# Kernel optimization log

Measured on AMD Instinct MI355X. Metric: run time of the kernel, lower is better.

Reference implementation:

```python
import jax, jax.numpy as jnp
import numpy as np

B, S, N, BS, D, H, V = 1, 2048, 128, 16, 512, 8, 32000
MASK_TOKEN_ID = 3


def setup_inputs() -> dict:
    key = jax.random.key(0)
    ks = jax.random.split(key, 10)
    anchors = jnp.sort(jax.random.randint(ks[0], (B, N), 0, S - BS), axis=1)
    return {
        "input_ids": jax.random.randint(ks[1], (B, S), 0, V),
        "hidden_states": jax.random.normal(ks[2], (B, S, D), dtype=jnp.float32),
        "loss_mask": jnp.ones((B, S), dtype=jnp.float32),
        "anchor_positions": anchors,
        "block_keep_mask": jnp.ones((B, N), dtype=bool),
        "embed_table": jax.random.normal(ks[3], (V, D), dtype=jnp.float32) * 0.02,
        "Wq": jax.random.normal(ks[4], (D, D), dtype=jnp.float32) * 0.02,
        "Wk": jax.random.normal(ks[5], (D, D), dtype=jnp.float32) * 0.02,
        "Wv": jax.random.normal(ks[6], (D, D), dtype=jnp.float32) * 0.02,
        "Wo": jax.random.normal(ks[7], (D, D), dtype=jnp.float32) * 0.02,
        "W_lm": jax.random.normal(ks[8], (D, V), dtype=jnp.float32) * 0.02,
    }


def dflash_sdpa_mask(anchor_positions, block_keep_mask):
    # KV layout: [context S | block_0 .. block_{N-1}], Q layout: [block_0 .. block_{N-1}]
    Q = N * BS
    KV = S + N * BS
    q_idx = jnp.arange(Q)              # [Q]
    kv_idx = jnp.arange(KV)            # [KV]
    q_blk = q_idx // BS                # [Q]
    anchor_q = anchor_positions[:, q_blk]          # [B,Q] anchor of each query's block
    keep_q = block_keep_mask[:, q_blk]             # [B,Q]
    is_ctx = kv_idx < S                             # [KV]
    mask_context = is_ctx[None, None, :] & (kv_idx[None, None, :] < anchor_q[:, :, None])  # [B,Q,KV]
    kv_blk = (kv_idx - S) // BS
    mask_draft = (kv_idx >= S)[None, :] & (q_blk[:, None] == kv_blk[None, :])              # [Q,KV]
    final = (mask_context | mask_draft[None]) & keep_q[:, :, None]                          # [B,Q,KV]
    return final


def reference(input_ids, hidden_states, loss_mask, anchor_positions, block_keep_mask,
              embed_table, Wq, Wk, Wv, Wo, W_lm):
    dh = D // H
    Q = N * BS

    # --- noise embedding: MASK token everywhere, anchor token at each block start ---
    safe_anchor = jnp.clip(anchor_positions, 0, S - 1)                     # [B,N]
    anchor_tokens = jnp.take_along_axis(input_ids, safe_anchor, axis=1)    # [B,N]
    start_tokens = jnp.where(block_keep_mask, anchor_tokens, MASK_TOKEN_ID)
    noise_ids = jnp.full((B, Q), MASK_TOKEN_ID, dtype=input_ids.dtype)
    noise_ids = noise_ids.at[:, jnp.arange(N) * BS].set(start_tokens)
    noise_embedding = embed_table[noise_ids]                               # [B,Q,D]

    # --- draft attention: Q = draft tokens, KV = [context hiddens | draft tokens] ---
    kv_in = jnp.concatenate([hidden_states, noise_embedding], axis=1)      # [B,S+Q,D]
    q = (noise_embedding @ Wq).reshape(B, Q, H, dh)
    k = (kv_in @ Wk).reshape(B, S + Q, H, dh)
    v = (kv_in @ Wv).reshape(B, S + Q, H, dh)
    scores = jnp.einsum("bqhd,bkhd->bhqk", q, k) / jnp.sqrt(jnp.float32(dh))
    mask = dflash_sdpa_mask(anchor_positions, block_keep_mask)[:, None]    # [B,1,Q,KV]
    attn = jax.nn.softmax(jnp.where(mask, scores, -1e9), axis=-1)
    out = jnp.einsum("bhqk,bkhd->bqhd", attn, v).reshape(B, Q, D) @ Wo     # [B,Q,D]
    logits = out @ W_lm                                                    # [B,Q,V]

    # --- block-wise CE loss ---
    offs = jnp.arange(BS)
    label_idx = anchor_positions[:, :, None] + offs[None, None, :]         # [B,N,BS]
    valid_label = label_idx < S
    safe_idx = jnp.clip(label_idx, 0, S - 1)
    ids_b = jnp.broadcast_to(input_ids[:, None, :], (B, N, S))
    target_ids = jnp.take_along_axis(ids_b, safe_idx, axis=2)              # [B,N,BS]
    lm_b = jnp.broadcast_to(loss_mask[:, None, :], (B, N, S))
    lm_g = jnp.take_along_axis(lm_b, safe_idx, axis=2)
    weight = (block_keep_mask[:, :, None].astype(jnp.float32)
              * valid_label.astype(jnp.float32)
              * (offs > 0)[None, None, :].astype(jnp.float32)
              * lm_g)                                                      # [B,N,BS]

    flat_logits = logits.reshape(-1, V)
    flat_targets = target_ids.reshape(-1)
    flat_w = weight.reshape(-1)
    logp = jax.nn.log_softmax(flat_logits, axis=-1)
    loss_per = -jnp.take_along_axis(logp, flat_targets[:, None], axis=1)[:, 0]
    loss = jnp.sum(loss_per * flat_w) / (jnp.sum(flat_w) + 1e-6)

    pred = jnp.argmax(flat_logits, axis=-1)
    correct = (pred == flat_targets) & (flat_w > 0.5)
    accuracy = jnp.sum(correct).astype(jnp.float32) / (jnp.sum(flat_w) + 1e-6)
    return loss, accuracy
```

## Files before the change

### kernel.cpp

```cpp
#include <hip/hip_runtime.h>

typedef unsigned short u16;
typedef __attribute__((ext_vector_type(4))) float f32x4;
typedef __attribute__((ext_vector_type(8))) short short8;
typedef __attribute__((ext_vector_type(4))) unsigned int uv4;
typedef __attribute__((ext_vector_type(4))) float fv4;
typedef __attribute__((ext_vector_type(4))) unsigned short usv4;

#define S_LEN 2048
#define NBLK 128
#define DMODEL 512
#define VOCAB 32000
#define QLEN 2048
#define KVLEN 4096
#define NSPLIT 250

#define GAS(p) ((const __attribute__((address_space(1))) void*)(const void*)(p))
#define LAS(p) ((__attribute__((address_space(3))) void*)(void*)(p))

__device__ __forceinline__ float bf2f(u16 u){
  union { unsigned int i; float f; } x; x.i = ((unsigned int)u) << 16; return x.f;
}
__device__ __forceinline__ u16 f2bf(float f){
  union { float f; unsigned int i; } x; x.f = f;
  unsigned int r = x.i + 0x7fffu + ((x.i >> 16) & 1u);
  return (u16)(r >> 16);
}

__global__ __launch_bounds__(256) void transpose4(const float* __restrict__ i0, const float* __restrict__ i1,
                                                  const float* __restrict__ i2, const float* __restrict__ i3,
                                                  u16* __restrict__ o0, u16* __restrict__ o1,
                                                  u16* __restrict__ o2, u16* __restrict__ o3){
  const float* in; u16* out;
  switch (blockIdx.z){
    case 0: in = i0; out = o0; break;
    case 1: in = i1; out = o1; break;
    case 2: in = i2; out = o2; break;
    default: in = i3; out = o3; break;
  }
  __shared__ float tile[32][33];
  int t = threadIdx.x, tx = t & 31, ty = t >> 5;
  int nb = blockIdx.x * 32, kb = blockIdx.y * 32;
  #pragma unroll
  for (int i = 0; i < 4; i++){
    int r = ty + i * 8;
    tile[r][tx] = in[(size_t)(kb + r) * 512 + nb + tx];
  }
  __syncthreads();
  #pragma unroll
  for (int i = 0; i < 4; i++){
    int r = ty + i * 8;
    out[(size_t)(nb + r) * 512 + kb + tx] = f2bf(tile[tx][r]);
  }
}

__global__ __launch_bounds__(256) void transpose_wlm_frag(const float* __restrict__ in,
                                                          u16* __restrict__ Wf){
  __shared__ float tile[32][33];
  int t = threadIdx.x, tx = t & 31, ty = t >> 5;
  int vb32 = blockIdx.x, kt = blockIdx.y;
  #pragma unroll
  for (int i = 0; i < 4; i++){
    int r = ty + i * 8;
    tile[r][tx] = in[(size_t)(kt * 32 + r) * VOCAB + vb32 * 32 + tx];
  }
  __syncthreads();
  int v_local = t >> 3, gg = t & 7;
  int g = gg >> 1, j0 = (gg & 1) * 4;
  int v = vb32 * 32 + v_local;
  int v16 = v >> 4, li = v & 15;
  usv4 o;
  #pragma unroll
  for (int jj = 0; jj < 4; jj++)
    o[jj] = f2bf(tile[g * 8 + j0 + jj][v_local]);
  *(usv4*)&Wf[(size_t)(((v16 * 16 + kt) * 64) + g * 16 + li) * 8 + j0] = o;
}

__global__ __launch_bounds__(128) void build_kv(const float* __restrict__ hidden,
                                                const float* __restrict__ embed,
                                                const int* __restrict__ input_ids,
                                                const int* __restrict__ anchors,
                                                const unsigned char* __restrict__ keep,
                                                u16* __restrict__ kvb){
  int row = blockIdx.x;
  int t = threadIdx.x;
  const float* src;
  if (row < S_LEN){
    src = hidden + (size_t)row * DMODEL;
  } else {
    int q = row - S_LEN;
    int id = 3;
    if ((q & 15) == 0){
      int n = q >> 4;
      if (keep[n]){
        int a = anchors[n]; a = min(max(a, 0), S_LEN - 1);
        id = input_ids[a];
      }
    }
    src = embed + (size_t)id * DMODEL;
  }
  int c = t * 4;
  fv4 v = *(const fv4*)&src[c];
  usv4 o; o[0] = f2bf(v[0]); o[1] = f2bf(v[1]); o[2] = f2bf(v[2]); o[3] = f2bf(v[3]);
  *(usv4*)&kvb[(size_t)row * DMODEL + c] = o;
}

__global__ __launch_bounds__(256) void qkv_gemm(const u16* __restrict__ kvb,
                                                const u16* __restrict__ WkT,
                                                const u16* __restrict__ WvT,
                                                const u16* __restrict__ WqT,
                                                u16* __restrict__ kb,
                                                u16* __restrict__ vTb,
                                                u16* __restrict__ qb2){
  __shared__ __align__(16) u16 As[2][128 * 64];
  __shared__ __align__(16) u16 Bs[2][64 * 64];
  int id = blockIdx.x;
  const u16* A = kvb; const u16* BT; u16* C; int ldc; int trans = 0;
  int rowbase, colbase;
  if (id < 256){
    BT = WkT; C = kb; ldc = 512;
    rowbase = (id & 31) * 128; colbase = (id >> 5) * 64;
  } else if (id < 512){
    int j = id - 256;
    BT = WvT; C = vTb; ldc = KVLEN; trans = 1;
    rowbase = (j & 31) * 128; colbase = (j >> 5) * 64;
  } else {
    int j = id - 512;
    A = kvb + (size_t)S_LEN * DMODEL;
    BT = WqT; C = qb2; ldc = 512;
    rowbase = (j & 15) * 128; colbase = (j >> 4) * 64;
  }
  int t = threadIdx.x, w = t >> 6, lane = t & 63;
  int g = lane >> 4, li = lane & 15;
  int r0 = t >> 3, cg0 = t & 7;
  int swz = (cg0 ^ (r0 & 7)) << 3;

  auto stageA = [&](u16* dst, int kb_){
    #pragma unroll
    for (int i = 0; i < 4; i++)
      __builtin_amdgcn_global_load_lds(GAS(&A[(size_t)(rowbase + r0 + i * 32) * DMODEL + kb_ + swz]),
                                       LAS(dst + i * 2048 + w * 512), 16, 0, 0);
  };
  auto stageB = [&](u16* dst, int kb_){
    #pragma unroll
    for (int i = 0; i < 2; i++)
      __builtin_amdgcn_global_load_lds(GAS(&BT[(size_t)(colbase + r0 + i * 32) * DMODEL + kb_ + swz]),
                                       LAS(dst + i * 2048 + w * 512), 16, 0, 0);
  };

  f32x4 acc[2][4];
  #pragma unroll
  for (int i = 0; i < 2; i++)
    #pragma unroll
    for (int j = 0; j < 4; j++)
      acc[i][j] = (f32x4){0.f, 0.f, 0.f, 0.f};

  stageA(As[0], 0); stageB(Bs[0], 0);

  for (int kt = 0; kt < 8; kt++){
    u16* curA = As[kt & 1]; u16* curB = Bs[kt & 1];
    if (kt < 7){
      stageA(As[(kt + 1) & 1], (kt + 1) * 64); stageB(Bs[(kt + 1) & 1], (kt + 1) * 64);
      asm volatile("s_waitcnt vmcnt(6)" ::: "memory");
    } else {
      asm volatile("s_waitcnt vmcnt(0)" ::: "memory");
    }
    __builtin_amdgcn_s_barrier();
    #pragma unroll
    for (int ks = 0; ks < 2; ks++){
      short8 af[2], bf[4];
      #pragma unroll
      for (int mf = 0; mf < 2; mf++){
        int row = w * 32 + mf * 16 + li;
        af[mf] = *(const short8*)&curA[row * 64 + (((ks * 4 + g) ^ (li & 7)) << 3)];
      }
      #pragma unroll
      for (int nf = 0; nf < 4; nf++){
        int row = nf * 16 + li;
        bf[nf] = *(const short8*)&curB[row * 64 + (((ks * 4 + g) ^ (li & 7)) << 3)];
      }
      #pragma unroll
      for (int mf = 0; mf < 2; mf++)
        #pragma unroll
        for (int nf = 0; nf < 4; nf++)
          acc[mf][nf] = __builtin_amdgcn_mfma_f32_16x16x32_bf16(af[mf], bf[nf], acc[mf][nf], 0, 0, 0);
    }
    __builtin_amdgcn_s_barrier();
  }

  #pragma unroll
  for (int mf = 0; mf < 2; mf++)
    #pragma unroll
    for (int nf = 0; nf < 4; nf++)
      #pragma unroll
      for (int r = 0; r < 4; r++){
        int row = rowbase + w * 32 + mf * 16 + g * 4 + r;
        int col = colbase + nf * 16 + li;
        u16 vv = f2bf(acc[mf][nf][r]);
        if (trans) C[(size_t)col * ldc + row] = vv;
        else       C[(size_t)row * ldc + col] = vv;
      }
}

__global__ __launch_bounds__(256) void gemmO(const u16* __restrict__ A,
                                             const u16* __restrict__ BT,
                                             u16* __restrict__ C){
  __shared__ __align__(16) u16 As[2][128 * 64];
  __shared__ __align__(16) u16 Bs[2][64 * 64];
  int t = threadIdx.x, w = t >> 6, lane = t & 63;
  int g = lane >> 4, li = lane & 15;
  int rowbase = blockIdx.x * 128, colbase = blockIdx.y * 64;
  int r0 = t >> 3, cg0 = t & 7;
  int swz = (cg0 ^ (r0 & 7)) << 3;

  auto stageA = [&](u16* dst, int kb_){
    #pragma unroll
    for (int i = 0; i < 4; i++)
      __builtin_amdgcn_global_load_lds(GAS(&A[(size_t)(rowbase + r0 + i * 32) * DMODEL + kb_ + swz]),
                                       LAS(dst + i * 2048 + w * 512), 16, 0, 0);
  };
  auto stageB = [&](u16* dst, int kb_){
    #pragma unroll
    for (int i = 0; i < 2; i++)
      __builtin_amdgcn_global_load_lds(GAS(&BT[(size_t)(colbase + r0 + i * 32) * DMODEL + kb_ + swz]),
                                       LAS(dst + i * 2048 + w * 512), 16, 0, 0);
  };

  f32x4 acc[2][4];
  #pragma unroll
  for (int i = 0; i < 2; i++)
    #pragma unroll
    for (int j = 0; j < 4; j++)
      acc[i][j] = (f32x4){0.f, 0.f, 0.f, 0.f};

  stageA(As[0], 0); stageB(Bs[0], 0);

  for (int kt = 0; kt < 8; kt++){
    u16* curA = As[kt & 1]; u16* curB = Bs[kt & 1];
    if (kt < 7){
      stageA(As[(kt + 1) & 1], (kt + 1) * 64); stageB(Bs[(kt + 1) & 1], (kt + 1) * 64);
      asm volatile("s_waitcnt vmcnt(6)" ::: "memory");
    } else {
      asm volatile("s_waitcnt vmcnt(0)" ::: "memory");
    }
    __builtin_amdgcn_s_barrier();
    #pragma unroll
    for (int ks = 0; ks < 2; ks++){
      short8 af[2], bf[4];
      #pragma unroll
      for (int mf = 0; mf < 2; mf++){
        int row = w * 32 + mf * 16 + li;
        af[mf] = *(const short8*)&curA[row * 64 + (((ks * 4 + g) ^ (li & 7)) << 3)];
      }
      #pragma unroll
      for (int nf = 0; nf < 4; nf++){
        int row = nf * 16 + li;
        bf[nf] = *(const short8*)&curB[row * 64 + (((ks * 4 + g) ^ (li & 7)) << 3)];
      }
      #pragma unroll
      for (int mf = 0; mf < 2; mf++)
        #pragma unroll
        for (int nf = 0; nf < 4; nf++)
          acc[mf][nf] = __builtin_amdgcn_mfma_f32_16x16x32_bf16(af[mf], bf[nf], acc[mf][nf], 0, 0, 0);
    }
    __builtin_amdgcn_s_barrier();
  }

  #pragma unroll
  for (int mf = 0; mf < 2; mf++)
    #pragma unroll
    for (int nf = 0; nf < 4; nf++)
      #pragma unroll
      for (int r = 0; r < 4; r++){
        int row = rowbase + w * 32 + mf * 16 + g * 4 + r;
        int col = colbase + nf * 16 + li;
        C[(size_t)row * DMODEL + col] = f2bf(acc[mf][nf][r]);
      }
}

__global__ __launch_bounds__(256) void attn_mfma(const u16* __restrict__ qb,
                                                 const u16* __restrict__ kb,
                                                 const u16* __restrict__ vT,
                                                 const int* __restrict__ anchors,
                                                 const unsigned char* __restrict__ keep,
                                                 u16* __restrict__ attnb){
  int n = blockIdx.x, h = blockIdx.y;
  int t = threadIdx.x, w = t >> 6, lane = t & 63;
  int g = lane >> 4, li = lane & 15;

  __shared__ __align__(16) u16 q_s[16][72];
  __shared__ __align__(16) u16 p_s[4][16][72];
  __shared__ float o_s[4][16][64];
  __shared__ float ml_s[4][2][16];

  {
    int r = t >> 4, c4 = (t & 15) * 4;
    *(usv4*)&q_s[r][c4] = *(const usv4*)&qb[(size_t)(n * 16 + r) * DMODEL + h * 64 + c4];
  }
  __syncthreads();

  int anchor = anchors[n];
  bool kp = keep[n] != 0;
  const u16* kh  = kb + h * 64;
  const u16* vTh = vT + (size_t)(h * 64) * KVLEN;

  if (!kp){
    if (w == 0){
      float acc = 0.f;
      const u16* row = vTh + (size_t)lane * KVLEN;
      for (int k2 = 0; k2 < KVLEN; k2 += 8){
        short8 vv = *(const short8*)&row[k2];
        #pragma unroll
        for (int j = 0; j < 8; j++) acc += bf2f((u16)vv[j]);
      }
      acc *= (1.f / 4096.f);
      u16 ov = f2bf(acc);
      for (int r = 0; r < 16; r++)
        attnb[(size_t)(n * 16 + r) * DMODEL + h * 64 + lane] = ov;
    }
    return;
  }

  short8 qa[2];
  #pragma unroll
  for (int ks = 0; ks < 2; ks++)
    qa[ks] = *(const short8*)&q_s[li][ks * 32 + g * 8];

  int nctx = (anchor + 63) >> 6;
  int ntot = nctx + 1;

  f32x4 o_acc[4];
  float m[4], l[4];
  #pragma unroll
  for (int i = 0; i < 4; i++){ o_acc[i] = (f32x4){0.f,0.f,0.f,0.f}; m[i] = -3e38f; l[i] = 0.f; }

  for (int c = w; c < ntot; c += 4){
    bool draft = (c == nctx);
    int kbase = draft ? (S_LEN + n * 16) : c * 64;
    int nk    = draft ? 16 : min(64, anchor - c * 64);

    f32x4 s[4];
    #pragma unroll
    for (int nf = 0; nf < 4; nf++) s[nf] = (f32x4){0.f,0.f,0.f,0.f};
    #pragma unroll
    for (int ks = 0; ks < 2; ks++){
      #pragma unroll
      for (int nf = 0; nf < 4; nf++){
        int krow = min(kbase + nf * 16 + li, KVLEN - 1);
        short8 bfrag = *(const short8*)&kh[(size_t)krow * DMODEL + ks * 32 + g * 8];
        s[nf] = __builtin_amdgcn_mfma_f32_16x16x32_bf16(qa[ks], bfrag, s[nf], 0, 0, 0);
      }
    }

    #pragma unroll
    for (int r = 0; r < 4; r++){
      float mx = -3e38f;
      #pragma unroll
      for (int nf = 0; nf < 4; nf++){
        float sv = s[nf][r] * 0.125f;
        if (nf * 16 + li >= nk) sv = -3e38f;
        s[nf][r] = sv;
        mx = fmaxf(mx, sv);
      }
      #pragma unroll
      for (int mm = 1; mm < 16; mm <<= 1) mx = fmaxf(mx, __shfl_xor(mx, mm));
      float mn = fmaxf(m[r], mx);
      float sc = __expf(m[r] - mn);
      float ps = 0.f;
      #pragma unroll
      for (int nf = 0; nf < 4; nf++){
        float p = __expf(s[nf][r] - mn);
        ps += p;
        p_s[w][g * 4 + r][nf * 16 + li] = f2bf(p);
      }
      #pragma unroll
      for (int mm = 1; mm < 16; mm <<= 1) ps += __shfl_xor(ps, mm);
      l[r] = l[r] * sc + ps;
      m[r] = mn;
      #pragma unroll
      for (int nfd = 0; nfd < 4; nfd++) o_acc[nfd][r] *= sc;
    }

    #pragma unroll
    for (int ks = 0; ks < 2; ks++){
      short8 pa = *(const short8*)&p_s[w][li][ks * 32 + g * 8];
      int kcol = min(kbase + ks * 32 + g * 8, KVLEN - 8);
      #pragma unroll
      for (int nfd = 0; nfd < 4; nfd++){
        short8 vfrag = *(const short8*)&vTh[(size_t)(nfd * 16 + li) * KVLEN + kcol];
        o_acc[nfd] = __builtin_amdgcn_mfma_f32_16x16x32_bf16(pa, vfrag, o_acc[nfd], 0, 0, 0);
      }
    }
  }

  #pragma unroll
  for (int r = 0; r < 4; r++){
    if (li == 0){ ml_s[w][0][g * 4 + r] = m[r]; ml_s[w][1][g * 4 + r] = l[r]; }
    #pragma unroll
    for (int nfd = 0; nfd < 4; nfd++)
      o_s[w][g * 4 + r][nfd * 16 + li] = o_acc[nfd][r];
  }
  __syncthreads();

  {
    int row = t >> 4, c0 = (t & 15) * 4;
    float M = -3e38f;
    #pragma unroll
    for (int ww = 0; ww < 4; ww++) M = fmaxf(M, ml_s[ww][0][row]);
    float L = 0.f, ew[4];
    #pragma unroll
    for (int ww = 0; ww < 4; ww++){
      ew[ww] = __expf(ml_s[ww][0][row] - M);
      L += ml_s[ww][1][row] * ew[ww];
    }
    float inv = 1.f / L;
    #pragma unroll
    for (int j = 0; j < 4; j++){
      float ov = 0.f;
      #pragma unroll
      for (int ww = 0; ww < 4; ww++) ov += o_s[ww][row][c0 + j] * ew[ww];
      attnb[(size_t)(n * 16 + row) * DMODEL + h * 64 + c0 + j] = f2bf(ov * inv);
    }
  }
}

__global__ __launch_bounds__(256) void lm_fused(const u16* __restrict__ obp,
                                                const u16* __restrict__ Wf,
                                                const int* __restrict__ input_ids,
                                                const int* __restrict__ anchors,
                                                float* __restrict__ pl,
                                                float* __restrict__ pt, float* __restrict__ pbv,
                                                int* __restrict__ pbi){
  __shared__ __align__(16) u16 Ob[2][128 * 32];
  __shared__ int tcol_s[128];

  int L = blockIdx.x;
  int T = (L & 7) * 500 + (L >> 3);
  int qbase = (T & 15) * 128;
  int vb = T >> 4;
  int vocabbase = vb * 128;
  int t = threadIdx.x, w = t >> 6, lane = t & 63;
  int g = lane >> 4, li = lane & 15;
  int wv = w & 1, wq = w >> 1;

  if (t < 128){
    int r = qbase + t; int n = r >> 4, off = r & 15;
    int lab = anchors[n] + off;
    int safe = min(max(lab, 0), S_LEN - 1);
    tcol_s[t] = input_ids[safe];
  }

  int sr = t >> 2;
  int scg = (t & 3) ^ ((sr >> 1) & 3);
  auto stageO = [&](u16* odst, int kt){
    #pragma unroll
    for (int i = 0; i < 2; i++)
      __builtin_amdgcn_global_load_lds(GAS(&obp[(size_t)(qbase + i * 64 + sr) * DMODEL + kt * 32 + (scg << 3)]),
                                       LAS(odst + i * 2048 + w * 512), 16, 0, 0);
  };
  const u16* wbase = Wf + ((size_t)(vb * 8 + wv * 4) * 16) * 512 + lane * 8;

  f32x4 acc[4][4];
  #pragma unroll
  for (int i = 0; i < 4; i++)
    #pragma unroll
    for (int j = 0; j < 4; j++)
      acc[i][j] = (f32x4){0.f, 0.f, 0.f, 0.f};

  stageO(Ob[0], 0);

  int cgr = (g ^ ((li >> 1) & 3)) << 3;
  for (int kt = 0; kt < 16; kt++){
    const u16* curO = Ob[kt & 1];
    short8 wfr[4];
    if (kt < 15){
      stageO(Ob[(kt + 1) & 1], kt + 1);
      #pragma unroll
      for (int vf = 0; vf < 4; vf++)
        wfr[vf] = *(const short8*)(wbase + ((size_t)(vf * 16 + kt) * 64) * 8);
      asm volatile("s_waitcnt vmcnt(6)" ::: "memory");
    } else {
      #pragma unroll
      for (int vf = 0; vf < 4; vf++)
        wfr[vf] = *(const short8*)(wbase + ((size_t)(vf * 16 + kt) * 64) * 8);
      asm volatile("s_waitcnt vmcnt(4)" ::: "memory");
    }
    __builtin_amdgcn_s_barrier();
    __builtin_amdgcn_s_setprio(1);
    short8 obf[4];
    #pragma unroll
    for (int qf = 0; qf < 4; qf++)
      obf[qf] = *(const short8*)&curO[(wq * 64 + qf * 16 + li) * 32 + cgr];
    #pragma unroll
    for (int vf = 0; vf < 4; vf++)
      #pragma unroll
      for (int qf = 0; qf < 4; qf++)
        acc[vf][qf] = __builtin_amdgcn_mfma_f32_16x16x32_bf16(wfr[vf], obf[qf], acc[vf][qf], 0, 0, 0);
    __builtin_amdgcn_s_setprio(0);
    __builtin_amdgcn_s_barrier();
  }
  __syncthreads();

  float* cse = (float*)&Ob[0][0];
  float* ctv = (float*)&Ob[0][512];
  float* cbv = (float*)&Ob[0][1024];
  int*   cbi = (int*)  &Ob[0][1536];

  #pragma unroll
  for (int qf = 0; qf < 4; qf++){
    int qloc = wq * 64 + qf * 16 + li;
    int tc = tcol_s[qloc] - (vocabbase + wv * 64);
    float se = 0.f, tv = -3e38f, bv = -3e38f; int bi = 0x7fffffff;
    #pragma unroll
    for (int vf = 0; vf < 4; vf++){
      #pragma unroll
      for (int r = 0; r < 4; r++){
        float v = acc[vf][qf][r];
        int pos = vf * 16 + g * 4 + r;
        se += __expf(v);
        if (pos == tc) tv = v;
        if (v > bv){ bv = v; bi = pos; }
      }
    }
    #pragma unroll
    for (int off = 16; off <= 32; off <<= 1){
      se += __shfl_xor(se, off);
      tv = fmaxf(tv, __shfl_xor(tv, off));
      float ob_ = __shfl_xor(bv, off); int oi = __shfl_xor(bi, off);
      if (ob_ > bv || (ob_ == bv && oi < bi)){ bv = ob_; bi = oi; }
    }
    if (g == 0){
      cse[wv * 128 + qloc] = se; ctv[wv * 128 + qloc] = tv;
      cbv[wv * 128 + qloc] = bv; cbi[wv * 128 + qloc] = wv * 64 + bi;
    }
  }
  __syncthreads();

  if (t < 128){
    float SE = 0.f, TV = -3e38f, BV = -3e38f; int BI = 0x7fffffff;
    #pragma unroll
    for (int vv = 0; vv < 2; vv++){
      SE += cse[vv * 128 + t];
      TV = fmaxf(TV, ctv[vv * 128 + t]);
      float v = cbv[vv * 128 + t];
      if (v > BV){ BV = v; BI = cbi[vv * 128 + t]; }
    }
    size_t idx = (size_t)vb * QLEN + qbase + t;
    pl[idx] = SE; pt[idx] = TV; pbv[idx] = BV; pbi[idx] = vocabbase + BI;
  }
}

__global__ __launch_bounds__(256) void loss_rows(const float* __restrict__ pl,
                                                 const float* __restrict__ pt, const float* __restrict__ pbv,
                                                 const int* __restrict__ pbi,
                                                 const int* __restrict__ input_ids,
                                                 const int* __restrict__ anchors,
                                                 const unsigned char* __restrict__ keep,
                                                 const float* __restrict__ loss_mask,
                                                 float* __restrict__ rowacc){
  int t = threadIdx.x, w = t >> 6, lane = t & 63;
  int row = blockIdx.x * 4 + w;
  float L = 0.f, TV = -3e38f, BV = -3e38f; int BI = 0x7fffffff;
  for (int s = lane; s < NSPLIT; s += 64){
    size_t idx = (size_t)s * QLEN + row;
    L += pl[idx];
    TV = fmaxf(TV, pt[idx]);
    float bv_ = pbv[idx]; int bi_ = pbi[idx];
    if (bv_ > BV || (bv_ == BV && bi_ < BI)){ BV = bv_; BI = bi_; }
  }
  #pragma unroll
  for (int mm = 1; mm < 64; mm <<= 1){
    L += __shfl_xor(L, mm);
    TV = fmaxf(TV, __shfl_xor(TV, mm));
    float ob = __shfl_xor(BV, mm); int oi = __shfl_xor(BI, mm);
    if (ob > BV || (ob == BV && oi < BI)){ BV = ob; BI = oi; }
  }
  if (lane == 0){
    int n = row >> 4, off = row & 15;
    int lab = anchors[n] + off;
    int valid = (lab < S_LEN) ? 1 : 0;
    int safe = min(max(lab, 0), S_LEN - 1);
    int tgt = input_ids[safe];
    float wgt = (keep[n] ? 1.f : 0.f) * (valid ? 1.f : 0.f) * ((off > 0) ? 1.f : 0.f) * loss_mask[safe];
    float logp = TV - __logf(L);
    rowacc[row * 3 + 0] = -logp * wgt;
    rowacc[row * 3 + 1] = wgt;
    rowacc[row * 3 + 2] = ((BI == tgt) && (wgt > 0.5f)) ? 1.f : 0.f;
  }
}

__global__ __launch_bounds__(256) void final_sum(const float* __restrict__ rowacc, float* __restrict__ out){
  int t = threadIdx.x;
  float a = 0.f, b = 0.f, c = 0.f;
  for (int r = t; r < QLEN; r += 256){
    a += rowacc[r * 3 + 0]; b += rowacc[r * 3 + 1]; c += rowacc[r * 3 + 2];
  }
  __shared__ float sa[256], sb[256], sc_[256];
  sa[t] = a; sb[t] = b; sc_[t] = c;
  __syncthreads();
  for (int s = 128; s >= 1; s >>= 1){
    if (t < s){ sa[t] += sa[t + s]; sb[t] += sb[t + s]; sc_[t] += sc_[t + s]; }
    __syncthreads();
  }
  if (t == 0){
    out[0] = sa[0] / (sb[0] + 1e-6f);
    out[1] = sc_[0] / (sb[0] + 1e-6f);
  }
}

extern "C" void kernel_launch(void* const* d_in, const int* in_sizes, int n_in,
                              void* d_out, int out_size, void* d_ws, size_t ws_size,
                              hipStream_t stream) {
  const int*   input_ids = (const int*)  d_in[0];
  const float* hidden    = (const float*)d_in[1];
  const float* loss_mask = (const float*)d_in[2];
  const int*   anchors   = (const int*)  d_in[3];
  const unsigned char* keep = (const unsigned char*)d_in[4];
  const float* embed     = (const float*)d_in[5];
  const float* Wq        = (const float*)d_in[6];
  const float* Wk        = (const float*)d_in[7];
  const float* Wv        = (const float*)d_in[8];
  const float* Wo        = (const float*)d_in[9];
  const float* Wlm       = (const float*)d_in[10];

  char* ws = (char*)d_ws;
  size_t off = 0;
  auto take = [&](size_t bytes) -> char* {
    char* p = ws + off;
    off += (bytes + 255) & ~(size_t)255;
    return p;
  };
  u16* WqT  = (u16*)take((size_t)512 * 512 * 2);
  u16* WkT  = (u16*)take((size_t)512 * 512 * 2);
  u16* WvT  = (u16*)take((size_t)512 * 512 * 2);
  u16* WoT  = (u16*)take((size_t)512 * 512 * 2);
  u16* Wfrag= (u16*)take((size_t)VOCAB * 512 * 2);
  u16* kvb  = (u16*)take((size_t)KVLEN * 512 * 2);
  u16* qb2  = (u16*)take((size_t)QLEN * 512 * 2);
  u16* kb   = (u16*)take((size_t)KVLEN * 512 * 2);
  u16* vTb  = (u16*)take((size_t)512 * KVLEN * 2);
  u16* attnb= (u16*)take((size_t)QLEN * 512 * 2);
  u16* ob   = (u16*)take((size_t)QLEN * 512 * 2);
  float* pl = (float*)take((size_t)QLEN * NSPLIT * 4);
  float* pt = (float*)take((size_t)QLEN * NSPLIT * 4);
  float* pbv= (float*)take((size_t)QLEN * NSPLIT * 4);
  int*   pbi= (int*)  take((size_t)QLEN * NSPLIT * 4);
  float* rowacc = (float*)take((size_t)QLEN * 3 * 4);

  transpose4<<<dim3(16, 16, 4), 256, 0, stream>>>(Wq, Wk, Wv, Wo, WqT, WkT, WvT, WoT);
  transpose_wlm_frag<<<dim3(1000, 16), 256, 0, stream>>>(Wlm, Wfrag);

  build_kv<<<KVLEN, 128, 0, stream>>>(hidden, embed, input_ids, anchors, keep, kvb);

  qkv_gemm<<<640, 256, 0, stream>>>(kvb, WkT, WvT, WqT, kb, vTb, qb2);

  attn_mfma<<<dim3(NBLK, 8), 256, 0, stream>>>(qb2, kb, vTb, anchors, keep, attnb);

  gemmO<<<dim3(16, 8), 256, 0, stream>>>(attnb, WoT, ob);

  lm_fused<<<4000, 256, 0, stream>>>(ob, Wfrag, input_ids, anchors, pl, pt, pbv, pbi);

  loss_rows<<<512, 256, 0, stream>>>(pl, pt, pbv, pbi, input_ids, anchors, keep, loss_mask, rowacc);

  final_sum<<<1, 256, 0, stream>>>(rowacc, (float*)d_out);
}
```

Measured before the change: 222.9 us.

## Double lm_fused K-tile depth, widen W_lm transpose stores, balance attention blocks

The LM-head GEMM now stages 64-wide K tiles of the output activations into LDS, using an 8-way XOR swizzle. This halves the number of barrier-separated iterations and doubles the MFMA work done between syncs, at the cost of more LDS and more in-flight weight registers. The W_lm fragment transpose handles 64 K-rows per block and writes 16-byte vectors per lane instead of 8-byte ones. Attention blocks are interleaved front-to-back so that blocks with short and long causal context mix and load balances better across CUs.

```diff
diff --git a/kernel.cpp b/kernel.cpp
--- a/kernel.cpp
+++ b/kernel.cpp
@@ -56,24 +56,25 @@
 
 __global__ __launch_bounds__(256) void transpose_wlm_frag(const float* __restrict__ in,
                                                           u16* __restrict__ Wf){
-  __shared__ float tile[32][33];
+  __shared__ float tile[64][33];
   int t = threadIdx.x, tx = t & 31, ty = t >> 5;
-  int vb32 = blockIdx.x, kt = blockIdx.y;
-  #pragma unroll
-  for (int i = 0; i < 4; i++){
+  int vb32 = blockIdx.x, kblk = blockIdx.y;
+  #pragma unroll
+  for (int i = 0; i < 8; i++){
     int r = ty + i * 8;
-    tile[r][tx] = in[(size_t)(kt * 32 + r) * VOCAB + vb32 * 32 + tx];
+    tile[r][tx] = in[(size_t)(kblk * 64 + r) * VOCAB + vb32 * 32 + tx];
   }
   __syncthreads();
-  int v_local = t >> 3, gg = t & 7;
-  int g = gg >> 1, j0 = (gg & 1) * 4;
-  int v = vb32 * 32 + v_local;
-  int v16 = v >> 4, li = v & 15;
-  usv4 o;
-  #pragma unroll
-  for (int jj = 0; jj < 4; jj++)
-    o[jj] = f2bf(tile[g * 8 + j0 + jj][v_local]);
-  *(usv4*)&Wf[(size_t)(((v16 * 16 + kt) * 64) + g * 16 + li) * 8 + j0] = o;
+  int w = t >> 6, lane = t & 63;
+  int v16sel = w & 1, ktsel = w >> 1;
+  int gsel = lane >> 4, li = lane & 15;
+  u16 tmp[8];
+  #pragma unroll
+  for (int j = 0; j < 8; j++)
+    tmp[j] = f2bf(tile[ktsel * 32 + gsel * 8 + j][v16sel * 16 + li]);
+  size_t v16 = vb32 * 2 + v16sel;
+  size_t kt32 = kblk * 2 + ktsel;
+  *(uv4*)&Wf[((v16 * 16 + kt32) * 64 + lane) * 8] = *(uv4*)tmp;
 }
 
 __global__ __launch_bounds__(128) void build_kv(const float* __restrict__ hidden,
@@ -284,7 +285,9 @@
                                                  const int* __restrict__ anchors,
                                                  const unsigned char* __restrict__ keep,
                                                  u16* __restrict__ attnb){
-  int n = blockIdx.x, h = blockIdx.y;
+  int bx = blockIdx.x;
+  int n = (bx & 1) ? (NBLK - 1 - (bx >> 1)) : (bx >> 1);
+  int h = blockIdx.y;
   int t = threadIdx.x, w = t >> 6, lane = t & 63;
   int g = lane >> 4, li = lane & 15;
 
@@ -431,7 +434,7 @@
                                                 float* __restrict__ pl,
                                                 float* __restrict__ pt, float* __restrict__ pbv,
                                                 int* __restrict__ pbi){
-  __shared__ __align__(16) u16 Ob[2][128 * 32];
+  __shared__ __align__(16) u16 Ob[2][128 * 64];
   __shared__ int tcol_s[128];
 
   int L = blockIdx.x;
@@ -450,12 +453,12 @@
     tcol_s[t] = input_ids[safe];
   }
 
-  int sr = t >> 2;
-  int scg = (t & 3) ^ ((sr >> 1) & 3);
+  int r0 = t >> 3, cg0 = t & 7;
+  int swz = (cg0 ^ (r0 & 7)) << 3;
   auto stageO = [&](u16* odst, int kt){
     #pragma unroll
-    for (int i = 0; i < 2; i++)
-      __builtin_amdgcn_global_load_lds(GAS(&obp[(size_t)(qbase + i * 64 + sr) * DMODEL + kt * 32 + (scg << 3)]),
+    for (int i = 0; i < 4; i++)
+      __builtin_amdgcn_global_load_lds(GAS(&obp[(size_t)(qbase + r0 + i * 32) * DMODEL + kt * 64 + swz]),
                                        LAS(odst + i * 2048 + w * 512), 16, 0, 0);
   };
   const u16* wbase = Wf + ((size_t)(vb * 8 + wv * 4) * 16) * 512 + lane * 8;
@@ -469,33 +472,39 @@
 
   stageO(Ob[0], 0);
 
-  int cgr = (g ^ ((li >> 1) & 3)) << 3;
-  for (int kt = 0; kt < 16; kt++){
+  for (int kt = 0; kt < 8; kt++){
     const u16* curO = Ob[kt & 1];
-    short8 wfr[4];
-    if (kt < 15){
+    short8 wfr[2][4];
+    if (kt < 7){
       stageO(Ob[(kt + 1) & 1], kt + 1);
       #pragma unroll
-      for (int vf = 0; vf < 4; vf++)
-        wfr[vf] = *(const short8*)(wbase + ((size_t)(vf * 16 + kt) * 64) * 8);
-      asm volatile("s_waitcnt vmcnt(6)" ::: "memory");
+      for (int ks = 0; ks < 2; ks++)
+        #pragma unroll
+        for (int vf = 0; vf < 4; vf++)
+          wfr[ks][vf] = *(const short8*)(wbase + ((size_t)(vf * 16 + kt * 2 + ks) * 64) * 8);
+      asm volatile("s_waitcnt vmcnt(12)" ::: "memory");
     } else {
       #pragma unroll
-      for (int vf = 0; vf < 4; vf++)
-        wfr[vf] = *(const short8*)(wbase + ((size_t)(vf * 16 + kt) * 64) * 8);
-      asm volatile("s_waitcnt vmcnt(4)" ::: "memory");
+      for (int ks = 0; ks < 2; ks++)
+        #pragma unroll
+        for (int vf = 0; vf < 4; vf++)
+          wfr[ks][vf] = *(const short8*)(wbase + ((size_t)(vf * 16 + kt * 2 + ks) * 64) * 8);
+      asm volatile("s_waitcnt vmcnt(8)" ::: "memory");
     }
     __builtin_amdgcn_s_barrier();
     __builtin_amdgcn_s_setprio(1);
-    short8 obf[4];
-    #pragma unroll
-    for (int qf = 0; qf < 4; qf++)
-      obf[qf] = *(const short8*)&curO[(wq * 64 + qf * 16 + li) * 32 + cgr];
-    #pragma unroll
-    for (int vf = 0; vf < 4; vf++)
+    #pragma unroll
+    for (int ks = 0; ks < 2; ks++){
+      short8 obf[4];
       #pragma unroll
       for (int qf = 0; qf < 4; qf++)
-        acc[vf][qf] = __builtin_amdgcn_mfma_f32_16x16x32_bf16(wfr[vf], obf[qf], acc[vf][qf], 0, 0, 0);
+        obf[qf] = *(const short8*)&curO[(wq * 64 + qf * 16 + li) * 64 + (((ks * 4 + g) ^ (li & 7)) << 3)];
+      #pragma unroll
+      for (int vf = 0; vf < 4; vf++)
+        #pragma unroll
+        for (int qf = 0; qf < 4; qf++)
+          acc[vf][qf] = __builtin_amdgcn_mfma_f32_16x16x32_bf16(wfr[ks][vf], obf[qf], acc[vf][qf], 0, 0, 0);
+    }
     __builtin_amdgcn_s_setprio(0);
     __builtin_amdgcn_s_barrier();
   }
@@ -648,7 +657,7 @@
   float* rowacc = (float*)take((size_t)QLEN * 3 * 4);
 
   transpose4<<<dim3(16, 16, 4), 256, 0, stream>>>(Wq, Wk, Wv, Wo, WqT, WkT, WvT, WoT);
-  transpose_wlm_frag<<<dim3(1000, 16), 256, 0, stream>>>(Wlm, Wfrag);
+  transpose_wlm_frag<<<dim3(1000, 8), 256, 0, stream>>>(Wlm, Wfrag);
 
   build_kv<<<KVLEN, 128, 0, stream>>>(hidden, embed, input_ids, anchors, keep, kvb);
 
```

Result: faster. 214.8 us (-3.6%).
